# Kernel optimization log

Hardware: AMD Instinct MI355X
Metric: run time of the kernel (lower is better)

Reference implementation:

```python
import jax, jax.numpy as jnp
import numpy as np

D_MODEL = 1024
N_HEADS = 16
HEAD_DIM = D_MODEL // N_HEADS
KV_LATENT = 512
N_EXPERTS = 4
D_HIDDEN = 4 * D_MODEL
B, T = 2, 1024


def rmsnorm(x, w, eps=1e-6):
    return w * (x * jax.lax.rsqrt(jnp.mean(x * x, axis=-1, keepdims=True) + eps))


def layernorm(x, g, b, eps=1e-5):
    mu = jnp.mean(x, axis=-1, keepdims=True)
    var = jnp.mean((x - mu) ** 2, axis=-1, keepdims=True)
    return (x - mu) * jax.lax.rsqrt(var + eps) * g + b


def apply_rope(x):
    # x: [b, h, t, d], half-split RoPE as in the torch source
    t, d = x.shape[2], x.shape[3]
    half = d // 2
    pos = jnp.arange(t, dtype=x.dtype)[:, None]                      # [t,1]
    inv_freq = 1.0 / (10000.0 ** (jnp.arange(half, dtype=x.dtype) / half))
    ang = pos * inv_freq[None, :]                                    # [t,half]
    sin, cos = jnp.sin(ang), jnp.cos(ang)
    x1, x2 = x[..., :half], x[..., half:]
    return jnp.concatenate([x1 * cos - x2 * sin, x1 * sin + x2 * cos], axis=-1)


def setup_inputs() -> dict:
    key = jax.random.key(0)
    ks = jax.random.split(key, 16)
    s = lambda fan_in: 1.0 / np.sqrt(fan_in)
    return {
        "x": jax.random.normal(ks[0], (B, T, D_MODEL), jnp.float32),
        "norm1_w": jnp.ones((D_MODEL,), jnp.float32),
        "norm2_w": jnp.ones((D_MODEL,), jnp.float32),
        "Wq": jax.random.normal(ks[1], (D_MODEL, D_MODEL), jnp.float32) * s(D_MODEL),
        "Wdkv": jax.random.normal(ks[2], (KV_LATENT, D_MODEL), jnp.float32) * s(D_MODEL),
        "Wuk": jax.random.normal(ks[3], (D_MODEL, KV_LATENT), jnp.float32) * s(KV_LATENT),
        "Wuv": jax.random.normal(ks[4], (D_MODEL, KV_LATENT), jnp.float32) * s(KV_LATENT),
        "Wo": jax.random.normal(ks[5], (D_MODEL, D_MODEL), jnp.float32) * s(D_MODEL),
        "ln_g": jnp.ones((KV_LATENT,), jnp.float32),
        "ln_b": jnp.zeros((KV_LATENT,), jnp.float32),
        "gate_w": jax.random.normal(ks[6], (N_EXPERTS, D_MODEL), jnp.float32) * s(D_MODEL),
        "gate_b": jnp.zeros((N_EXPERTS,), jnp.float32),
        "W1": jax.random.normal(ks[7], (N_EXPERTS, D_HIDDEN, D_MODEL), jnp.float32) * s(D_MODEL),
        "b1": jnp.zeros((N_EXPERTS, D_HIDDEN), jnp.float32),
        "W2": jax.random.normal(ks[8], (N_EXPERTS, D_MODEL, D_HIDDEN), jnp.float32) * s(D_HIDDEN),
        "b2": jnp.zeros((N_EXPERTS, D_MODEL), jnp.float32),
    }


def mla_attention(x, Wq, Wdkv, Wuk, Wuv, Wo, ln_g, ln_b):
    b, t, _ = x.shape
    q = (x @ Wq.T).reshape(b, t, N_HEADS, HEAD_DIM).transpose(0, 2, 1, 3)  # [b,h,t,dh]
    latent = layernorm(x @ Wdkv.T, ln_g, ln_b)                             # [b,t,L]
    k = (latent @ Wuk.T).reshape(b, t, N_HEADS, HEAD_DIM).transpose(0, 2, 1, 3)
    v = (latent @ Wuv.T).reshape(b, t, N_HEADS, HEAD_DIM).transpose(0, 2, 1, 3)
    q = apply_rope(q)
    k = apply_rope(k)
    scores = jnp.einsum("bhqd,bhkd->bhqk", q, k) / np.sqrt(HEAD_DIM)
    causal = jnp.tril(jnp.ones((t, t), dtype=bool))
    scores = jnp.where(causal, scores, -jnp.inf)
    attn = jax.nn.softmax(scores, axis=-1)  # dropout is identity in eval
    out = jnp.einsum("bhqk,bhkd->bhqd", attn, v).transpose(0, 2, 1, 3).reshape(b, t, D_MODEL)
    return out @ Wo.T


def moe(x, gate_w, gate_b, W1, b1, W2, b2):
    # top-1 routing: each token goes to exactly one expert (argmax of gate)
    logits = x @ gate_w.T + gate_b                                  # [b,t,E]
    top = jnp.argmax(logits, axis=-1)                               # [b,t]
    onehot = jax.nn.one_hot(top, N_EXPERTS, dtype=x.dtype)          # [b,t,E]
    h = jax.nn.relu(jnp.einsum("btd,ehd->bteh", x, W1) + b1)        # [b,t,E,H]
    y = jnp.einsum("bteh,edh->bted", h, W2) + b2                    # [b,t,E,D]
    return jnp.einsum("bted,bte->btd", y, onehot)


def reference(x, norm1_w, norm2_w, Wq, Wdkv, Wuk, Wuv, Wo, ln_g, ln_b,
              gate_w, gate_b, W1, b1, W2, b2):
    x = x + mla_attention(rmsnorm(x, norm1_w), Wq, Wdkv, Wuk, Wuv, Wo, ln_g, ln_b)
    x = x + moe(rmsnorm(x, norm2_w), gate_w, gate_b, W1, b1, W2, b2)
    return x
```

## Files before the change

### kernel.cpp

```cpp
#include <hip/hip_runtime.h>
#include <hip/hip_bf16.h>
#include <math.h>

typedef unsigned short u16;
typedef __attribute__((ext_vector_type(4))) float floatx4;
typedef __attribute__((ext_vector_type(8))) short shortx8;

#define DEVI static __device__ __forceinline__

DEVI u16 f2b(float f) {
  union { float f; unsigned int i; } v; v.f = f;
  unsigned int x = v.i;
  return (u16)((x + 0x7fffu + ((x >> 16) & 1u)) >> 16);
}

constexpr int T_ = 1024, D_ = 1024, HD_ = 64, KV_ = 512, DH_ = 4096, M_ = 2048;
#define NEGBIG (-1e30f)

__global__ __launch_bounds__(256) void k_rms1b(const float* __restrict__ x, const float* __restrict__ w,
                                               u16* __restrict__ outb) {
  int row = blockIdx.x, tid = threadIdx.x;
  float4 v = *(const float4*)&x[(size_t)row * D_ + tid * 4];
  float ss = v.x*v.x + v.y*v.y + v.z*v.z + v.w*v.w;
  #pragma unroll
  for (int m = 32; m >= 1; m >>= 1) ss += __shfl_xor(ss, m, 64);
  __shared__ float red[4];
  if ((tid & 63) == 0) red[tid >> 6] = ss;
  __syncthreads();
  ss = red[0] + red[1] + red[2] + red[3];
  float sc = 1.0f / sqrtf(ss * (1.0f / 1024.0f) + 1e-6f);
  float4 wv = *(const float4*)&w[tid * 4];
  ushort4 ob;
  ob.x = f2b(wv.x*v.x*sc); ob.y = f2b(wv.y*v.y*sc);
  ob.z = f2b(wv.z*v.z*sc); ob.w = f2b(wv.w*v.w*sc);
  *(ushort4*)&outb[(size_t)row * D_ + tid * 4] = ob;
}

__global__ __launch_bounds__(256) void k_rms2b(const float* __restrict__ x, const float* __restrict__ w,
                                               float* __restrict__ outf, u16* __restrict__ outb) {
  int row = blockIdx.x, tid = threadIdx.x;
  float4 v = *(const float4*)&x[(size_t)row * D_ + tid * 4];
  float ss = v.x*v.x + v.y*v.y + v.z*v.z + v.w*v.w;
  #pragma unroll
  for (int m = 32; m >= 1; m >>= 1) ss += __shfl_xor(ss, m, 64);
  __shared__ float red[4];
  if ((tid & 63) == 0) red[tid >> 6] = ss;
  __syncthreads();
  ss = red[0] + red[1] + red[2] + red[3];
  float sc = 1.0f / sqrtf(ss * (1.0f / 1024.0f) + 1e-6f);
  float4 wv = *(const float4*)&w[tid * 4];
  float4 o; o.x = wv.x*v.x*sc; o.y = wv.y*v.y*sc; o.z = wv.z*v.z*sc; o.w = wv.w*v.w*sc;
  *(float4*)&outf[(size_t)row * D_ + tid * 4] = o;
  ushort4 ob; ob.x = f2b(o.x); ob.y = f2b(o.y); ob.z = f2b(o.z); ob.w = f2b(o.w);
  *(ushort4*)&outb[(size_t)row * D_ + tid * 4] = ob;
}

__global__ __launch_bounds__(256) void k_lnb(const float* __restrict__ lat, const float* __restrict__ g,
                                             const float* __restrict__ bb, u16* __restrict__ ob) {
  int row = blockIdx.x, tid = threadIdx.x;
  const float* r = lat + (size_t)row * KV_;
  float v0 = r[tid], v1 = r[tid + 256];
  float s = v0 + v1;
  #pragma unroll
  for (int m = 32; m >= 1; m >>= 1) s += __shfl_xor(s, m, 64);
  __shared__ float red[4];
  if ((tid & 63) == 0) red[tid >> 6] = s;
  __syncthreads();
  float mu = (red[0] + red[1] + red[2] + red[3]) * (1.0f / 512.0f);
  __syncthreads();
  float d0 = v0 - mu, d1 = v1 - mu;
  float ss = d0*d0 + d1*d1;
  #pragma unroll
  for (int m = 32; m >= 1; m >>= 1) ss += __shfl_xor(ss, m, 64);
  if ((tid & 63) == 0) red[tid >> 6] = ss;
  __syncthreads();
  float var = (red[0] + red[1] + red[2] + red[3]) * (1.0f / 512.0f);
  float sc = 1.0f / sqrtf(var + 1e-5f);
  ob[(size_t)row * KV_ + tid]       = f2b(d0 * sc * g[tid]       + bb[tid]);
  ob[(size_t)row * KV_ + tid + 256] = f2b(d1 * sc * g[tid + 256] + bb[tid + 256]);
}

__global__ __launch_bounds__(256) void k_cvtall(const float* __restrict__ W1, const float* __restrict__ W2,
                                                const float* __restrict__ Wq, const float* __restrict__ Wdkv,
                                                const float* __restrict__ Wuk, const float* __restrict__ Wuv,
                                                const float* __restrict__ Wo, u16* __restrict__ dst) {
  for (size_t i = (size_t)blockIdx.x * 256 + threadIdx.x; i < 9306112ull; i += (size_t)gridDim.x * 256) {
    const float* s;
    if      (i < 4194304ull) s = W1   + i * 4;
    else if (i < 8388608ull) s = W2   + (i - 4194304ull) * 4;
    else if (i < 8650752ull) s = Wq   + (i - 8388608ull) * 4;
    else if (i < 8781824ull) s = Wdkv + (i - 8650752ull) * 4;
    else if (i < 8912896ull) s = Wuk  + (i - 8781824ull) * 4;
    else if (i < 9043968ull) s = Wuv  + (i - 8912896ull) * 4;
    else                     s = Wo   + (i - 9043968ull) * 4;
    float4 f = *(const float4*)s;
    ushort4 u; u.x = f2b(f.x); u.y = f2b(f.y); u.z = f2b(f.z); u.w = f2b(f.w);
    *(ushort4*)(dst + i * 4) = u;
  }
}

template<int BF16B>
__global__ __launch_bounds__(256) void k_gemm_t(const u16* __restrict__ A, const void* __restrict__ Bp,
                                                const float* __restrict__ resid, float* __restrict__ Cf,
                                                u16* __restrict__ Cb, int N, int K) {
  int bid = blockIdx.x;
  int xcd = bid & 7, jj = bid >> 3;
  int mt = jj & 31, nt = (jj >> 5) * 8 + xcd;
  __shared__ __align__(16) u16 As[64][72];
  __shared__ __align__(16) u16 Bs[64][72];
  int tid = threadIdx.x, lane = tid & 63, wave = tid >> 6;
  int wm = (wave >> 1) * 32, wn = (wave & 1) * 32;
  int lr = tid >> 2, lc = (tid & 3) * 16;
  const u16* arow = A + (size_t)(mt * 64 + lr) * K + lc;
  const u16* browb = (const u16*)Bp + (size_t)(nt * 64 + lr) * K + lc;
  const float* browf = (const float*)Bp + (size_t)(nt * 64 + lr) * K + lc;
  floatx4 z = {0.f, 0.f, 0.f, 0.f};
  floatx4 acc00 = z, acc01 = z, acc10 = z, acc11 = z;
  int fm = lane & 15, fkq = (lane >> 4) * 8;
  uint4 ra0 = *(const uint4*)&arow[0];
  uint4 ra1 = *(const uint4*)&arow[8];
  uint4 rbA, rbB; float4 rb0, rb1, rb2, rb3;
  if constexpr (BF16B) {
    rbA = *(const uint4*)&browb[0]; rbB = *(const uint4*)&browb[8];
  } else {
    rb0 = *(const float4*)&browf[0];  rb1 = *(const float4*)&browf[4];
    rb2 = *(const float4*)&browf[8];  rb3 = *(const float4*)&browf[12];
  }
  for (int kb = 0; kb < K; kb += 64) {
    *(uint4*)&As[lr][lc]     = ra0;
    *(uint4*)&As[lr][lc + 8] = ra1;
    if constexpr (BF16B) {
      *(uint4*)&Bs[lr][lc]     = rbA;
      *(uint4*)&Bs[lr][lc + 8] = rbB;
    } else {
      ushort4 u;
      u.x = f2b(rb0.x); u.y = f2b(rb0.y); u.z = f2b(rb0.z); u.w = f2b(rb0.w); *(ushort4*)&Bs[lr][lc]      = u;
      u.x = f2b(rb1.x); u.y = f2b(rb1.y); u.z = f2b(rb1.z); u.w = f2b(rb1.w); *(ushort4*)&Bs[lr][lc + 4]  = u;
      u.x = f2b(rb2.x); u.y = f2b(rb2.y); u.z = f2b(rb2.z); u.w = f2b(rb2.w); *(ushort4*)&Bs[lr][lc + 8]  = u;
      u.x = f2b(rb3.x); u.y = f2b(rb3.y); u.z = f2b(rb3.z); u.w = f2b(rb3.w); *(ushort4*)&Bs[lr][lc + 12] = u;
    }
    __syncthreads();
    if (kb + 64 < K) {
      ra0 = *(const uint4*)&arow[kb + 64];
      ra1 = *(const uint4*)&arow[kb + 72];
      if constexpr (BF16B) {
        rbA = *(const uint4*)&browb[kb + 64]; rbB = *(const uint4*)&browb[kb + 72];
      } else {
        rb0 = *(const float4*)&browf[kb + 64]; rb1 = *(const float4*)&browf[kb + 68];
        rb2 = *(const float4*)&browf[kb + 72]; rb3 = *(const float4*)&browf[kb + 76];
      }
    }
    #pragma unroll
    for (int ks = 0; ks < 64; ks += 32) {
      shortx8 a0  = *(const shortx8*)&As[wm + fm][ks + fkq];
      shortx8 a1  = *(const shortx8*)&As[wm + 16 + fm][ks + fkq];
      shortx8 b0  = *(const shortx8*)&Bs[wn + fm][ks + fkq];
      shortx8 b1v = *(const shortx8*)&Bs[wn + 16 + fm][ks + fkq];
      acc00 = __builtin_amdgcn_mfma_f32_16x16x32_bf16(a0, b0,  acc00, 0, 0, 0);
      acc01 = __builtin_amdgcn_mfma_f32_16x16x32_bf16(a0, b1v, acc01, 0, 0, 0);
      acc10 = __builtin_amdgcn_mfma_f32_16x16x32_bf16(a1, b0,  acc10, 0, 0, 0);
      acc11 = __builtin_amdgcn_mfma_f32_16x16x32_bf16(a1, b1v, acc11, 0, 0, 0);
    }
    __syncthreads();
  }
  int q4 = (lane >> 4) * 4, cix = lane & 15;
  #pragma unroll
  for (int im = 0; im < 2; ++im) {
    #pragma unroll
    for (int rg = 0; rg < 4; ++rg) {
      int row = mt * 64 + wm + im * 16 + q4 + rg;
      #pragma unroll
      for (int in = 0; in < 2; ++in) {
        int gn = nt * 64 + wn + in * 16 + cix;
        float vv = (im == 0 ? (in == 0 ? acc00[rg] : acc01[rg]) : (in == 0 ? acc10[rg] : acc11[rg]));
        size_t idx = (size_t)row * N + gn;
        if (Cb) {
          Cb[idx] = f2b(vv);
        } else {
          if (resid) vv += resid[idx];
          Cf[idx] = vv;
        }
      }
    }
  }
}

__global__ __launch_bounds__(256) void k_rope2b(const float* __restrict__ q, const float* __restrict__ k,
                                                u16* __restrict__ qb, u16* __restrict__ kb) {
  int g = blockIdx.x * 256 + threadIdx.x;
  int j = g & 31;
  int h = (g >> 5) & 15;
  int row = g >> 9;
  int t = row & (T_ - 1);
  float p = (float)pow(10000.0, (double)j * (1.0 / 32.0));
  float ang = (float)t / p;
  float sn, cs; sincosf(ang, &sn, &cs);
  size_t base = (size_t)row * D_ + h * 64 + j;
  float x1 = q[base], x2 = q[base + 32];
  qb[base]      = f2b((x1 * cs - x2 * sn) * 0.125f);
  qb[base + 32] = f2b((x1 * sn + x2 * cs) * 0.125f);
  x1 = k[base]; x2 = k[base + 32];
  kb[base]      = f2b(x1 * cs - x2 * sn);
  kb[base + 32] = f2b(x1 * sn + x2 * cs);
}

__global__ __launch_bounds__(256) void k_fattn(const u16* __restrict__ qbp, const u16* __restrict__ kbp,
                                               const u16* __restrict__ vbp, u16* __restrict__ ob) {
  int idx = blockIdx.x, h = blockIdx.y;
  int b = idx >> 4;
  int qt = idx & 15;
  if (b) qt = 15 - qt;
  __shared__ __align__(16) u16 Qs[64][72];
  __shared__ __align__(16) u16 Ks[64][72];
  __shared__ __align__(16) u16 Vs[64][72];
  __shared__ __align__(16) u16 Ps[64][72];
  __shared__ float red1[2][64];
  __shared__ float red2[2][64];
  int tid = threadIdx.x, lane = tid & 63, wave = tid >> 6;
  int wm = (wave >> 1) * 32, wn = (wave & 1) * 32, w1 = wave & 1;
  int fm = lane & 15, fkq = (lane >> 4) * 8;
  int q4 = (lane >> 4) * 4, cix = lane & 15;
  size_t rowbase = (size_t)b * T_;
  int colbase = h * HD_;
  int q0 = qt * 64;
  int lr = tid >> 2, ld = (tid & 3) * 16;
  {
    const u16* qr = qbp + (rowbase + q0 + lr) * D_ + colbase + ld;
    *(uint4*)&Qs[lr][ld]     = *(const uint4*)&qr[0];
    *(uint4*)&Qs[lr][ld + 8] = *(const uint4*)&qr[8];
  }
  floatx4 z = {0.f, 0.f, 0.f, 0.f};
  floatx4 s[2][2], o[2][2];
  o[0][0] = z; o[0][1] = z; o[1][0] = z; o[1][1] = z;
  float m[2][4], l[2][4], f_[2][4];
  #pragma unroll
  for (int im = 0; im < 2; ++im)
    #pragma unroll
    for (int rg = 0; rg < 4; ++rg) { m[im][rg] = NEGBIG; l[im][rg] = 0.f; }
  for (int kt = 0; kt <= qt; ++kt) {
    __syncthreads();
    {
      const u16* kr = kbp + (rowbase + kt * 64 + lr) * D_ + colbase + ld;
      *(uint4*)&Ks[lr][ld]     = *(const uint4*)&kr[0];
      *(uint4*)&Ks[lr][ld + 8] = *(const uint4*)&kr[8];
      const u16* vr = vbp + (rowbase + kt * 64 + lr) * D_ + colbase + ld;
      #pragma unroll
      for (int c = 0; c < 16; ++c) Vs[ld + c][lr] = vr[c];
    }
    __syncthreads();
    s[0][0] = z; s[0][1] = z; s[1][0] = z; s[1][1] = z;
    #pragma unroll
    for (int ks = 0; ks < 64; ks += 32) {
      shortx8 a0  = *(const shortx8*)&Qs[wm + fm][ks + fkq];
      shortx8 a1  = *(const shortx8*)&Qs[wm + 16 + fm][ks + fkq];
      shortx8 b0  = *(const shortx8*)&Ks[wn + fm][ks + fkq];
      shortx8 b1v = *(const shortx8*)&Ks[wn + 16 + fm][ks + fkq];
      s[0][0] = __builtin_amdgcn_mfma_f32_16x16x32_bf16(a0, b0,  s[0][0], 0, 0, 0);
      s[0][1] = __builtin_amdgcn_mfma_f32_16x16x32_bf16(a0, b1v, s[0][1], 0, 0, 0);
      s[1][0] = __builtin_amdgcn_mfma_f32_16x16x32_bf16(a1, b0,  s[1][0], 0, 0, 0);
      s[1][1] = __builtin_amdgcn_mfma_f32_16x16x32_bf16(a1, b1v, s[1][1], 0, 0, 0);
    }
    if (kt == qt) {
      #pragma unroll
      for (int im = 0; im < 2; ++im)
        #pragma unroll
        for (int rg = 0; rg < 4; ++rg) {
          int r = wm + im * 16 + q4 + rg;
          #pragma unroll
          for (int in = 0; in < 2; ++in)
            if (wn + in * 16 + cix > r) s[im][in][rg] = NEGBIG;
        }
    }
    #pragma unroll
    for (int im = 0; im < 2; ++im)
      #pragma unroll
      for (int rg = 0; rg < 4; ++rg) {
        float pm = fmaxf(s[im][0][rg], s[im][1][rg]);
        #pragma unroll
        for (int mk = 8; mk >= 1; mk >>= 1) pm = fmaxf(pm, __shfl_xor(pm, mk, 64));
        if (cix == 0) red1[w1][wm + im * 16 + q4 + rg] = pm;
        f_[im][rg] = pm;
      }
    __syncthreads();
    #pragma unroll
    for (int im = 0; im < 2; ++im)
      #pragma unroll
      for (int rg = 0; rg < 4; ++rg) {
        int r = wm + im * 16 + q4 + rg;
        float mx = fmaxf(f_[im][rg], red1[w1 ^ 1][r]);
        float mn = fmaxf(m[im][rg], mx);
        float f = __expf(m[im][rg] - mn);
        m[im][rg] = mn;
        float p0 = __expf(s[im][0][rg] - mn);
        float p1 = __expf(s[im][1][rg] - mn);
        float ss = p0 + p1;
        #pragma unroll
        for (int mk = 8; mk >= 1; mk >>= 1) ss += __shfl_xor(ss, mk, 64);
        if (cix == 0) red2[w1][r] = ss;
        Ps[r][wn + cix]      = f2b(p0);
        Ps[r][wn + 16 + cix] = f2b(p1);
        l[im][rg] *= f;
        o[im][0][rg] *= f;
        o[im][1][rg] *= f;
      }
    __syncthreads();
    #pragma unroll
    for (int im = 0; im < 2; ++im)
      #pragma unroll
      for (int rg = 0; rg < 4; ++rg) {
        int r = wm + im * 16 + q4 + rg;
        l[im][rg] += red2[0][r] + red2[1][r];
      }
    #pragma unroll
    for (int ks = 0; ks < 64; ks += 32) {
      shortx8 a0  = *(const shortx8*)&Ps[wm + fm][ks + fkq];
      shortx8 a1  = *(const shortx8*)&Ps[wm + 16 + fm][ks + fkq];
      shortx8 b0  = *(const shortx8*)&Vs[wn + fm][ks + fkq];
      shortx8 b1v = *(const shortx8*)&Vs[wn + 16 + fm][ks + fkq];
      o[0][0] = __builtin_amdgcn_mfma_f32_16x16x32_bf16(a0, b0,  o[0][0], 0, 0, 0);
      o[0][1] = __builtin_amdgcn_mfma_f32_16x16x32_bf16(a0, b1v, o[0][1], 0, 0, 0);
      o[1][0] = __builtin_amdgcn_mfma_f32_16x16x32_bf16(a1, b0,  o[1][0], 0, 0, 0);
      o[1][1] = __builtin_amdgcn_mfma_f32_16x16x32_bf16(a1, b1v, o[1][1], 0, 0, 0);
    }
  }
  #pragma unroll
  for (int im = 0; im < 2; ++im)
    #pragma unroll
    for (int rg = 0; rg < 4; ++rg) {
      int r = wm + im * 16 + q4 + rg;
      float inv = 1.0f / l[im][rg];
      size_t base = (rowbase + q0 + r) * D_ + colbase;
      ob[base + wn + cix]      = f2b(o[im][0][rg] * inv);
      ob[base + wn + 16 + cix] = f2b(o[im][1][rg] * inv);
    }
}

__global__ __launch_bounds__(256) void k_init(int* cnt) { if (threadIdx.x < 4) cnt[threadIdx.x] = 0; }

__global__ __launch_bounds__(256) void k_gate(const float* __restrict__ h2, const float* __restrict__ gw,
                                              const float* __restrict__ gb, int* __restrict__ expert,
                                              int* __restrict__ cnt) {
  int wid = threadIdx.x >> 6, lane = threadIdx.x & 63;
  int t = blockIdx.x * 4 + wid;
  const float* hr = h2 + (size_t)t * D_;
  float a0 = 0, a1 = 0, a2 = 0, a3 = 0;
  for (int c = lane; c < D_; c += 64) {
    float xv = hr[c];
    a0 += xv * gw[c];
    a1 += xv * gw[D_ + c];
    a2 += xv * gw[2 * D_ + c];
    a3 += xv * gw[3 * D_ + c];
  }
  #pragma unroll
  for (int m = 32; m >= 1; m >>= 1) {
    a0 += __shfl_xor(a0, m, 64); a1 += __shfl_xor(a1, m, 64);
    a2 += __shfl_xor(a2, m, 64); a3 += __shfl_xor(a3, m, 64);
  }
  if (lane == 0) {
    float l0 = a0 + gb[0], l1 = a1 + gb[1], l2 = a2 + gb[2], l3 = a3 + gb[3];
    int best = 0; float bv = l0;
    if (l1 > bv) { bv = l1; best = 1; }
    if (l2 > bv) { bv = l2; best = 2; }
    if (l3 > bv) { bv = l3; best = 3; }
    expert[t] = best;
    atomicAdd(&cnt[best], 1);
  }
}

__global__ __launch_bounds__(256) void k_scatter(const int* __restrict__ expert, const int* __restrict__ cnt,
                                                 int* __restrict__ off, int* __restrict__ sorted) {
  __shared__ int cur[4];
  if (threadIdx.x == 0) {
    int o0 = 0, o1 = cnt[0], o2 = o1 + cnt[1], o3 = o2 + cnt[2];
    off[0] = o0; off[1] = o1; off[2] = o2; off[3] = o3;
    cur[0] = o0; cur[1] = o1; cur[2] = o2; cur[3] = o3;
  }
  __syncthreads();
  for (int t = threadIdx.x; t < M_; t += 256) {
    int e = expert[t];
    int p = atomicAdd(&cur[e], 1);
    sorted[p] = t;
  }
}

template<int BF16B>
__global__ __launch_bounds__(256) void k_moe1_t(const u16* __restrict__ A, const void* __restrict__ W1p,
                                                const float* __restrict__ b1, const int* __restrict__ cnt,
                                                const int* __restrict__ off, const int* __restrict__ sorted,
                                                u16* __restrict__ hbuf) {
  int bid = blockIdx.x;
  int xcd = bid & 7, jj = bid >> 3;
  int mt = jj & 31, combo = (jj >> 5) * 8 + xcd;
  int e = combo >> 6, nt = combo & 63;
  int rem = cnt[e] - mt * 64;
  if (rem <= 0) return;
  __shared__ __align__(16) u16 As[64][72];
  __shared__ __align__(16) u16 Bs[64][72];
  int tid = threadIdx.x, lane = tid & 63, wave = tid >> 6;
  int wm = (wave >> 1) * 32, wn = (wave & 1) * 32;
  int lr = tid >> 2, lc = (tid & 3) * 16;
  int rr = lr < rem ? lr : rem - 1;
  const u16* arow = A + (size_t)sorted[off[e] + mt * 64 + rr] * D_ + lc;
  const u16* browb = (const u16*)W1p + (size_t)e * DH_ * D_ + (size_t)(nt * 64 + lr) * D_ + lc;
  const float* browf = (const float*)W1p + (size_t)e * DH_ * D_ + (size_t)(nt * 64 + lr) * D_ + lc;
  floatx4 z = {0.f, 0.f, 0.f, 0.f};
  floatx4 acc00 = z, acc01 = z, acc10 = z, acc11 = z;
  int fm = lane & 15, fkq = (lane >> 4) * 8;
  uint4 ra0 = *(const uint4*)&arow[0];
  uint4 ra1 = *(const uint4*)&arow[8];
  uint4 rbA, rbB; float4 rb0, rb1, rb2, rb3;
  if constexpr (BF16B) {
    rbA = *(const uint4*)&browb[0]; rbB = *(const uint4*)&browb[8];
  } else {
    rb0 = *(const float4*)&browf[0];  rb1 = *(const float4*)&browf[4];
    rb2 = *(const float4*)&browf[8];  rb3 = *(const float4*)&browf[12];
  }
  for (int kb = 0; kb < D_; kb += 64) {
    *(uint4*)&As[lr][lc]     = ra0;
    *(uint4*)&As[lr][lc + 8] = ra1;
    if constexpr (BF16B) {
      *(uint4*)&Bs[lr][lc]     = rbA;
      *(uint4*)&Bs[lr][lc + 8] = rbB;
    } else {
      ushort4 u;
      u.x = f2b(rb0.x); u.y = f2b(rb0.y); u.z = f2b(rb0.z); u.w = f2b(rb0.w); *(ushort4*)&Bs[lr][lc]      = u;
      u.x = f2b(rb1.x); u.y = f2b(rb1.y); u.z = f2b(rb1.z); u.w = f2b(rb1.w); *(ushort4*)&Bs[lr][lc + 4]  = u;
      u.x = f2b(rb2.x); u.y = f2b(rb2.y); u.z = f2b(rb2.z); u.w = f2b(rb2.w); *(ushort4*)&Bs[lr][lc + 8]  = u;
      u.x = f2b(rb3.x); u.y = f2b(rb3.y); u.z = f2b(rb3.z); u.w = f2b(rb3.w); *(ushort4*)&Bs[lr][lc + 12] = u;
    }
    __syncthreads();
    if (kb + 64 < D_) {
      ra0 = *(const uint4*)&arow[kb + 64];
      ra1 = *(const uint4*)&arow[kb + 72];
      if constexpr (BF16B) {
        rbA = *(const uint4*)&browb[kb + 64]; rbB = *(const uint4*)&browb[kb + 72];
      } else {
        rb0 = *(const float4*)&browf[kb + 64]; rb1 = *(const float4*)&browf[kb + 68];
        rb2 = *(const float4*)&browf[kb + 72]; rb3 = *(const float4*)&browf[kb + 76];
      }
    }
    #pragma unroll
    for (int ks = 0; ks < 64; ks += 32) {
      shortx8 a0  = *(const shortx8*)&As[wm + fm][ks + fkq];
      shortx8 a1  = *(const shortx8*)&As[wm + 16 + fm][ks + fkq];
      shortx8 b0  = *(const shortx8*)&Bs[wn + fm][ks + fkq];
      shortx8 b1v = *(const shortx8*)&Bs[wn + 16 + fm][ks + fkq];
      acc00 = __builtin_amdgcn_mfma_f32_16x16x32_bf16(a0, b0,  acc00, 0, 0, 0);
      acc01 = __builtin_amdgcn_mfma_f32_16x16x32_bf16(a0, b1v, acc01, 0, 0, 0);
      acc10 = __builtin_amdgcn_mfma_f32_16x16x32_bf16(a1, b0,  acc10, 0, 0, 0);
      acc11 = __builtin_amdgcn_mfma_f32_16x16x32_bf16(a1, b1v, acc11, 0, 0, 0);
    }
    __syncthreads();
  }
  int q4 = (lane >> 4) * 4, cix = lane & 15;
  #pragma unroll
  for (int im = 0; im < 2; ++im) {
    #pragma unroll
    for (int rg = 0; rg < 4; ++rg) {
      int ml = wm + im * 16 + q4 + rg;
      if (ml >= rem) continue;
      size_t grow = (size_t)(off[e] + mt * 64 + ml);
      #pragma unroll
      for (int in = 0; in < 2; ++in) {
        int gn = nt * 64 + wn + in * 16 + cix;
        float vv = (im == 0 ? (in == 0 ? acc00[rg] : acc01[rg]) : (in == 0 ? acc10[rg] : acc11[rg]));
        vv += b1[e * DH_ + gn];
        hbuf[grow * DH_ + gn] = f2b(fmaxf(vv, 0.f));
      }
    }
  }
}

template<int BF16B>
__global__ __launch_bounds__(256) void k_moe2_t(const u16* __restrict__ hbuf, const void* __restrict__ W2p,
                                                const float* __restrict__ b2w, const float* __restrict__ x1f,
                                                const int* __restrict__ cnt, const int* __restrict__ off,
                                                const int* __restrict__ sorted, float* __restrict__ out) {
  int bid = blockIdx.x;
  int xcd = bid & 7, jj = bid >> 3;
  int mt = jj & 31, combo = (jj >> 5) * 8 + xcd;
  int e = combo >> 4, nt = combo & 15;
  int rem = cnt[e] - mt * 64;
  if (rem <= 0) return;
  __shared__ __align__(16) u16 As[64][72];
  __shared__ __align__(16) u16 Bs[64][72];
  int tid = threadIdx.x, lane = tid & 63, wave = tid >> 6;
  int wm = (wave >> 1) * 32, wn = (wave & 1) * 32;
  int lr = tid >> 2, lc = (tid & 3) * 16;
  int rr = lr < rem ? lr : rem - 1;
  const u16* arow = hbuf + (size_t)(off[e] + mt * 64 + rr) * DH_ + lc;
  const u16* browb = (const u16*)W2p + (size_t)e * D_ * DH_ + (size_t)(nt * 64 + lr) * DH_ + lc;
  const float* browf = (const float*)W2p + (size_t)e * D_ * DH_ + (size_t)(nt * 64 + lr) * DH_ + lc;
  floatx4 z = {0.f, 0.f, 0.f, 0.f};
  floatx4 acc00 = z, acc01 = z, acc10 = z, acc11 = z;
  int fm = lane & 15, fkq = (lane >> 4) * 8;
  uint4 ra0 = *(const uint4*)&arow[0];
  uint4 ra1 = *(const uint4*)&arow[8];
  uint4 rbA, rbB; float4 rb0, rb1, rb2, rb3;
  if constexpr (BF16B) {
    rbA = *(const uint4*)&browb[0]; rbB = *(const uint4*)&browb[8];
  } else {
    rb0 = *(const float4*)&browf[0];  rb1 = *(const float4*)&browf[4];
    rb2 = *(const float4*)&browf[8];  rb3 = *(const float4*)&browf[12];
  }
  for (int kb = 0; kb < DH_; kb += 64) {
    *(uint4*)&As[lr][lc]     = ra0;
    *(uint4*)&As[lr][lc + 8] = ra1;
    if constexpr (BF16B) {
      *(uint4*)&Bs[lr][lc]     = rbA;
      *(uint4*)&Bs[lr][lc + 8] = rbB;
    } else {
      ushort4 u;
      u.x = f2b(rb0.x); u.y = f2b(rb0.y); u.z = f2b(rb0.z); u.w = f2b(rb0.w); *(ushort4*)&Bs[lr][lc]      = u;
      u.x = f2b(rb1.x); u.y = f2b(rb1.y); u.z = f2b(rb1.z); u.w = f2b(rb1.w); *(ushort4*)&Bs[lr][lc + 4]  = u;
      u.x = f2b(rb2.x); u.y = f2b(rb2.y); u.z = f2b(rb2.z); u.w = f2b(rb2.w); *(ushort4*)&Bs[lr][lc + 8]  = u;
      u.x = f2b(rb3.x); u.y = f2b(rb3.y); u.z = f2b(rb3.z); u.w = f2b(rb3.w); *(ushort4*)&Bs[lr][lc + 12] = u;
    }
    __syncthreads();
    if (kb + 64 < DH_) {
      ra0 = *(const uint4*)&arow[kb + 64];
      ra1 = *(const uint4*)&arow[kb + 72];
      if constexpr (BF16B) {
        rbA = *(const uint4*)&browb[kb + 64]; rbB = *(const uint4*)&browb[kb + 72];
      } else {
        rb0 = *(const float4*)&browf[kb + 64]; rb1 = *(const float4*)&browf[kb + 68];
        rb2 = *(const float4*)&browf[kb + 72]; rb3 = *(const float4*)&browf[kb + 76];
      }
    }
    #pragma unroll
    for (int ks = 0; ks < 64; ks += 32) {
      shortx8 a0  = *(const shortx8*)&As[wm + fm][ks + fkq];
      shortx8 a1  = *(const shortx8*)&As[wm + 16 + fm][ks + fkq];
      shortx8 b0  = *(const shortx8*)&Bs[wn + fm][ks + fkq];
      shortx8 b1v = *(const shortx8*)&Bs[wn + 16 + fm][ks + fkq];
      acc00 = __builtin_amdgcn_mfma_f32_16x16x32_bf16(a0, b0,  acc00, 0, 0, 0);
      acc01 = __builtin_amdgcn_mfma_f32_16x16x32_bf16(a0, b1v, acc01, 0, 0, 0);
      acc10 = __builtin_amdgcn_mfma_f32_16x16x32_bf16(a1, b0,  acc10, 0, 0, 0);
      acc11 = __builtin_amdgcn_mfma_f32_16x16x32_bf16(a1, b1v, acc11, 0, 0, 0);
    }
    __syncthreads();
  }
  int q4 = (lane >> 4) * 4, cix = lane & 15;
  #pragma unroll
  for (int im = 0; im < 2; ++im) {
    #pragma unroll
    for (int rg = 0; rg < 4; ++rg) {
      int ml = wm + im * 16 + q4 + rg;
      if (ml >= rem) continue;
      int tok = sorted[off[e] + mt * 64 + ml];
      #pragma unroll
      for (int in = 0; in < 2; ++in) {
        int gn = nt * 64 + wn + in * 16 + cix;
        float vv = (im == 0 ? (in == 0 ? acc00[rg] : acc01[rg]) : (in == 0 ? acc10[rg] : acc11[rg]));
        out[(size_t)tok * D_ + gn] = vv + b2w[e * D_ + gn] + x1f[(size_t)tok * D_ + gn];
      }
    }
  }
}

__global__ __launch_bounds__(256) void k_moe2s(const u16* __restrict__ hbuf, const u16* __restrict__ W2b,
                                               const int* __restrict__ cnt, const int* __restrict__ off,
                                               float* __restrict__ pbuf) {
  int bid = blockIdx.x;
  int xcd = bid & 7, jj = bid >> 3;
  int mt = jj & 31;
  int combo = (jj >> 5) * 8 + xcd;
  int ks = combo & 1, ec = combo >> 1;
  int e = ec >> 4, nt = ec & 15;
  int rem = cnt[e] - mt * 64;
  if (rem <= 0) return;
  const int KS = DH_ / 2;
  int k0 = ks * KS;
  __shared__ __align__(16) u16 As[64][72];
  __shared__ __align__(16) u16 Bs[64][72];
  int tid = threadIdx.x, lane = tid & 63, wave = tid >> 6;
  int wm = (wave >> 1) * 32, wn = (wave & 1) * 32;
  int lr = tid >> 2, lc = (tid & 3) * 16;
  int rr = lr < rem ? lr : rem - 1;
  const u16* arow = hbuf + (size_t)(off[e] + mt * 64 + rr) * DH_ + k0 + lc;
  const u16* brow = W2b + (size_t)e * D_ * DH_ + (size_t)(nt * 64 + lr) * DH_ + k0 + lc;
  floatx4 z = {0.f, 0.f, 0.f, 0.f};
  floatx4 acc00 = z, acc01 = z, acc10 = z, acc11 = z;
  int fm = lane & 15, fkq = (lane >> 4) * 8;
  uint4 ra0 = *(const uint4*)&arow[0];
  uint4 ra1 = *(const uint4*)&arow[8];
  uint4 rbA = *(const uint4*)&brow[0];
  uint4 rbB = *(const uint4*)&brow[8];
  for (int kb = 0; kb < KS; kb += 64) {
    *(uint4*)&As[lr][lc]     = ra0;
    *(uint4*)&As[lr][lc + 8] = ra1;
    *(uint4*)&Bs[lr][lc]     = rbA;
    *(uint4*)&Bs[lr][lc + 8] = rbB;
    __syncthreads();
    if (kb + 64 < KS) {
      ra0 = *(const uint4*)&arow[kb + 64];
      ra1 = *(const uint4*)&arow[kb + 72];
      rbA = *(const uint4*)&brow[kb + 64];
      rbB = *(const uint4*)&brow[kb + 72];
    }
    #pragma unroll
    for (int kk = 0; kk < 64; kk += 32) {
      shortx8 a0  = *(const shortx8*)&As[wm + fm][kk + fkq];
      shortx8 a1  = *(const shortx8*)&As[wm + 16 + fm][kk + fkq];
      shortx8 b0  = *(const shortx8*)&Bs[wn + fm][kk + fkq];
      shortx8 b1v = *(const shortx8*)&Bs[wn + 16 + fm][kk + fkq];
      acc00 = __builtin_amdgcn_mfma_f32_16x16x32_bf16(a0, b0,  acc00, 0, 0, 0);
      acc01 = __builtin_amdgcn_mfma_f32_16x16x32_bf16(a0, b1v, acc01, 0, 0, 0);
      acc10 = __builtin_amdgcn_mfma_f32_16x16x32_bf16(a1, b0,  acc10, 0, 0, 0);
      acc11 = __builtin_amdgcn_mfma_f32_16x16x32_bf16(a1, b1v, acc11, 0, 0, 0);
    }
    __syncthreads();
  }
  float* pb = pbuf + (size_t)ks * M_ * D_;
  int q4 = (lane >> 4) * 4, cix = lane & 15;
  #pragma unroll
  for (int im = 0; im < 2; ++im) {
    #pragma unroll
    for (int rg = 0; rg < 4; ++rg) {
      int ml = wm + im * 16 + q4 + rg;
      if (ml >= rem) continue;
      size_t srow = (size_t)(off[e] + mt * 64 + ml);
      #pragma unroll
      for (int in = 0; in < 2; ++in) {
        int gn = nt * 64 + wn + in * 16 + cix;
        float vv = (im == 0 ? (in == 0 ? acc00[rg] : acc01[rg]) : (in == 0 ? acc10[rg] : acc11[rg]));
        pb[srow * D_ + gn] = vv;
      }
    }
  }
}

__global__ __launch_bounds__(256) void k_moered(const float* __restrict__ pbuf, const float* __restrict__ b2w,
                                                const float* __restrict__ x1f, const int* __restrict__ off,
                                                const int* __restrict__ sorted, float* __restrict__ out) {
  int r = blockIdx.x, tid = threadIdx.x;
  int tok = sorted[r];
  int e = (r >= off[3]) ? 3 : (r >= off[2]) ? 2 : (r >= off[1]) ? 1 : 0;
  size_t c = (size_t)tid * 4;
  float4 a = *(const float4*)&pbuf[(size_t)r * D_ + c];
  float4 b = *(const float4*)&pbuf[(size_t)M_ * D_ + (size_t)r * D_ + c];
  float4 bb = *(const float4*)&b2w[(size_t)e * D_ + c];
  float4 xr = *(const float4*)&x1f[(size_t)tok * D_ + c];
  float4 o;
  o.x = a.x + b.x + bb.x + xr.x;
  o.y = a.y + b.y + bb.y + xr.y;
  o.z = a.z + b.z + bb.z + xr.z;
  o.w = a.w + b.w + bb.w + xr.w;
  *(float4*)&out[(size_t)tok * D_ + c] = o;
}

extern "C" void kernel_launch(void* const* d_in, const int* in_sizes, int n_in,
                              void* d_out, int out_size, void* d_ws, size_t ws_size,
                              hipStream_t stream) {
  int map[16];
  for (int i = 0; i < 16; ++i) map[i] = i;
  if (n_in == 16 && in_sizes[0] == 16777216) {
    const int mm[16] = {15, 13, 14, 4, 2, 5, 6, 3, 12, 11, 10, 9, 0, 7, 1, 8};
    for (int i = 0; i < 16; ++i) map[i] = mm[i];
  } else if (n_in == 16 && in_sizes[0] == 4096) {
    for (int i = 0; i < 16; ++i) map[i] = 15 - i;
  }
  const float* x    = (const float*)d_in[map[0]];
  const float* n1w  = (const float*)d_in[map[1]];
  const float* n2w  = (const float*)d_in[map[2]];
  const float* Wq   = (const float*)d_in[map[3]];
  const float* Wdkv = (const float*)d_in[map[4]];
  const float* Wuk  = (const float*)d_in[map[5]];
  const float* Wuv  = (const float*)d_in[map[6]];
  const float* Wo   = (const float*)d_in[map[7]];
  const float* lng  = (const float*)d_in[map[8]];
  const float* lnb  = (const float*)d_in[map[9]];
  const float* gw   = (const float*)d_in[map[10]];
  const float* gb   = (const float*)d_in[map[11]];
  const float* W1   = (const float*)d_in[map[12]];
  const float* b1   = (const float*)d_in[map[13]];
  const float* W2   = (const float*)d_in[map[14]];
  const float* b2w  = (const float*)d_in[map[15]];
  float* out = (float*)d_out;
  char* ws = (char*)d_ws;
  const size_t MB = 1ull << 20;
  float* qf   = (float*)(ws + 0);
  float* x1f  = (float*)(ws + 0);
  float* kf   = (float*)(ws + 8 * MB);
  u16*   hbuf = (u16*)(ws + 8 * MB);
  float* latf = (float*)(ws + 16 * MB);
  u16*   qb   = (u16*)(ws + 16 * MB);
  u16*   h1b  = (u16*)(ws + 20 * MB);
  u16*   kb   = (u16*)(ws + 20 * MB);
  u16*   latb = (u16*)(ws + 24 * MB);
  float* h2f  = (float*)(ws + 24 * MB);
  u16*   vb   = (u16*)(ws + 26 * MB);
  u16*   ab   = (u16*)(ws + 30 * MB);
  u16*   h2b  = (u16*)(ws + 32 * MB);
  float* pbuf = (float*)(ws + 24 * MB);

  bool big = ws_size >= (107ull * MB + (64ull << 10));
  u16* wb = (u16*)(ws + 36 * MB);
  u16* W1b   = wb;
  u16* W2b   = wb + 16777216;
  u16* Wqb   = wb + 33554432;
  u16* Wdkvb = wb + 34603008;
  u16* Wukb  = wb + 35127296;
  u16* Wuvb  = wb + 35651584;
  u16* Wob   = wb + 36175872;
  int* cnt    = (int*)(ws + (big ? 107 * MB : 36 * MB));
  int* off    = cnt + 8;
  int* expert = cnt + 16;
  int* sorted = expert + 2048;

  if (big) {
    k_cvtall<<<2048, 256, 0, stream>>>(W1, W2, Wq, Wdkv, Wuk, Wuv, Wo, wb);
    k_rms1b<<<2048, 256, 0, stream>>>(x, n1w, h1b);
    k_gemm_t<1><<<512, 256, 0, stream>>>(h1b, Wqb, nullptr, qf, nullptr, 1024, 1024);
    k_gemm_t<1><<<256, 256, 0, stream>>>(h1b, Wdkvb, nullptr, latf, nullptr, 512, 1024);
    k_lnb<<<2048, 256, 0, stream>>>(latf, lng, lnb, latb);
    k_gemm_t<1><<<512, 256, 0, stream>>>(latb, Wukb, nullptr, kf, nullptr, 1024, 512);
    k_gemm_t<1><<<512, 256, 0, stream>>>(latb, Wuvb, nullptr, nullptr, vb, 1024, 512);
    k_rope2b<<<4096, 256, 0, stream>>>(qf, kf, qb, kb);
    k_fattn<<<dim3(32, 16), 256, 0, stream>>>(qb, kb, vb, ab);
    k_gemm_t<1><<<512, 256, 0, stream>>>(ab, Wob, x, x1f, nullptr, 1024, 1024);
    k_rms2b<<<2048, 256, 0, stream>>>(x1f, n2w, h2f, h2b);
    k_init<<<1, 64, 0, stream>>>(cnt);
    k_gate<<<512, 256, 0, stream>>>(h2f, gw, gb, expert, cnt);
    k_scatter<<<1, 256, 0, stream>>>(expert, cnt, off, sorted);
    k_moe1_t<1><<<8192, 256, 0, stream>>>(h2b, W1b, b1, cnt, off, sorted, hbuf);
    k_moe2s<<<4096, 256, 0, stream>>>(hbuf, W2b, cnt, off, pbuf);
    k_moered<<<2048, 256, 0, stream>>>(pbuf, b2w, x1f, off, sorted, out);
  } else {
    k_rms1b<<<2048, 256, 0, stream>>>(x, n1w, h1b);
    k_gemm_t<0><<<512, 256, 0, stream>>>(h1b, Wq, nullptr, qf, nullptr, 1024, 1024);
    k_gemm_t<0><<<256, 256, 0, stream>>>(h1b, Wdkv, nullptr, latf, nullptr, 512, 1024);
    k_lnb<<<2048, 256, 0, stream>>>(latf, lng, lnb, latb);
    k_gemm_t<0><<<512, 256, 0, stream>>>(latb, Wuk, nullptr, kf, nullptr, 1024, 512);
    k_gemm_t<0><<<512, 256, 0, stream>>>(latb, Wuv, nullptr, nullptr, vb, 1024, 512);
    k_rope2b<<<4096, 256, 0, stream>>>(qf, kf, qb, kb);
    k_fattn<<<dim3(32, 16), 256, 0, stream>>>(qb, kb, vb, ab);
    k_gemm_t<0><<<512, 256, 0, stream>>>(ab, Wo, x, x1f, nullptr, 1024, 1024);
    k_rms2b<<<2048, 256, 0, stream>>>(x1f, n2w, h2f, h2b);
    k_init<<<1, 64, 0, stream>>>(cnt);
    k_gate<<<512, 256, 0, stream>>>(h2f, gw, gb, expert, cnt);
    k_scatter<<<1, 256, 0, stream>>>(expert, cnt, off, sorted);
    k_moe1_t<0><<<8192, 256, 0, stream>>>(h2b, W1, b1, cnt, off, sorted, hbuf);
    k_moe2_t<0><<<2048, 256, 0, stream>>>(hbuf, W2, b2w, x1f, cnt, off, sorted, out);
  }
}
```

Baseline: 468.7 us.

## Give each wave full key rows in flash attention and prefetch K/V

Changes the flash-attention warp split so each of the four waves owns 16 query rows across all 64 keys, instead of a 2x2 quadrant split. Row max and row sum now come from in-wave shuffles alone, which removes the shared-memory reduction buffers and two block-wide barriers per key tile. Global K/V loads for the next tile are issued into registers before the current tile's compute, overlapping memory latency with MFMA work. The cost is more registers per thread for the prefetched tile, and the V transpose into shared memory now happens from registers.

```diff
diff --git a/kernel.cpp b/kernel.cpp
--- a/kernel.cpp
+++ b/kernel.cpp
@@ -214,12 +214,10 @@
   __shared__ __align__(16) u16 Ks[64][72];
   __shared__ __align__(16) u16 Vs[64][72];
   __shared__ __align__(16) u16 Ps[64][72];
-  __shared__ float red1[2][64];
-  __shared__ float red2[2][64];
   int tid = threadIdx.x, lane = tid & 63, wave = tid >> 6;
-  int wm = (wave >> 1) * 32, wn = (wave & 1) * 32, w1 = wave & 1;
   int fm = lane & 15, fkq = (lane >> 4) * 8;
   int q4 = (lane >> 4) * 4, cix = lane & 15;
+  int w16 = wave * 16;
   size_t rowbase = (size_t)b * T_;
   int colbase = h * HD_;
   int q0 = qt * 64;
@@ -230,109 +228,89 @@
     *(uint4*)&Qs[lr][ld + 8] = *(const uint4*)&qr[8];
   }
   floatx4 z = {0.f, 0.f, 0.f, 0.f};
-  floatx4 s[2][2], o[2][2];
-  o[0][0] = z; o[0][1] = z; o[1][0] = z; o[1][1] = z;
-  float m[2][4], l[2][4], f_[2][4];
-  #pragma unroll
-  for (int im = 0; im < 2; ++im)
-    #pragma unroll
-    for (int rg = 0; rg < 4; ++rg) { m[im][rg] = NEGBIG; l[im][rg] = 0.f; }
+  floatx4 s[4], o[4];
+  o[0] = z; o[1] = z; o[2] = z; o[3] = z;
+  float m[4], l[4];
+  #pragma unroll
+  for (int rg = 0; rg < 4; ++rg) { m[rg] = NEGBIG; l[rg] = 0.f; }
+  const u16* kr = kbp + (rowbase + lr) * D_ + colbase + ld;
+  const u16* vr = vbp + (rowbase + lr) * D_ + colbase + ld;
+  uint4 rk0 = *(const uint4*)&kr[0], rk1 = *(const uint4*)&kr[8];
+  uint4 rv0 = *(const uint4*)&vr[0], rv1 = *(const uint4*)&vr[8];
   for (int kt = 0; kt <= qt; ++kt) {
     __syncthreads();
+    *(uint4*)&Ks[lr][ld]     = rk0;
+    *(uint4*)&Ks[lr][ld + 8] = rk1;
     {
-      const u16* kr = kbp + (rowbase + kt * 64 + lr) * D_ + colbase + ld;
-      *(uint4*)&Ks[lr][ld]     = *(const uint4*)&kr[0];
-      *(uint4*)&Ks[lr][ld + 8] = *(const uint4*)&kr[8];
-      const u16* vr = vbp + (rowbase + kt * 64 + lr) * D_ + colbase + ld;
-      #pragma unroll
-      for (int c = 0; c < 16; ++c) Vs[ld + c][lr] = vr[c];
-    }
-    __syncthreads();
-    s[0][0] = z; s[0][1] = z; s[1][0] = z; s[1][1] = z;
+      union { uint4 v4[2]; u16 e[16]; } vv;
+      vv.v4[0] = rv0; vv.v4[1] = rv1;
+      #pragma unroll
+      for (int c = 0; c < 16; ++c) Vs[ld + c][lr] = vv.e[c];
+    }
+    __syncthreads();
+    if (kt < qt) {
+      kr += 64 * D_; vr += 64 * D_;
+      rk0 = *(const uint4*)&kr[0]; rk1 = *(const uint4*)&kr[8];
+      rv0 = *(const uint4*)&vr[0]; rv1 = *(const uint4*)&vr[8];
+    }
+    s[0] = z; s[1] = z; s[2] = z; s[3] = z;
     #pragma unroll
     for (int ks = 0; ks < 64; ks += 32) {
-      shortx8 a0  = *(const shortx8*)&Qs[wm + fm][ks + fkq];
-      shortx8 a1  = *(const shortx8*)&Qs[wm + 16 + fm][ks + fkq];
-      shortx8 b0  = *(const shortx8*)&Ks[wn + fm][ks + fkq];
-      shortx8 b1v = *(const shortx8*)&Ks[wn + 16 + fm][ks + fkq];
-      s[0][0] = __builtin_amdgcn_mfma_f32_16x16x32_bf16(a0, b0,  s[0][0], 0, 0, 0);
-      s[0][1] = __builtin_amdgcn_mfma_f32_16x16x32_bf16(a0, b1v, s[0][1], 0, 0, 0);
-      s[1][0] = __builtin_amdgcn_mfma_f32_16x16x32_bf16(a1, b0,  s[1][0], 0, 0, 0);
-      s[1][1] = __builtin_amdgcn_mfma_f32_16x16x32_bf16(a1, b1v, s[1][1], 0, 0, 0);
+      shortx8 a = *(const shortx8*)&Qs[w16 + fm][ks + fkq];
+      #pragma unroll
+      for (int nb = 0; nb < 4; ++nb) {
+        shortx8 bb = *(const shortx8*)&Ks[nb * 16 + fm][ks + fkq];
+        s[nb] = __builtin_amdgcn_mfma_f32_16x16x32_bf16(a, bb, s[nb], 0, 0, 0);
+      }
     }
     if (kt == qt) {
       #pragma unroll
-      for (int im = 0; im < 2; ++im)
+      for (int nb = 0; nb < 4; ++nb)
         #pragma unroll
-        for (int rg = 0; rg < 4; ++rg) {
-          int r = wm + im * 16 + q4 + rg;
-          #pragma unroll
-          for (int in = 0; in < 2; ++in)
-            if (wn + in * 16 + cix > r) s[im][in][rg] = NEGBIG;
-        }
-    }
-    #pragma unroll
-    for (int im = 0; im < 2; ++im)
-      #pragma unroll
-      for (int rg = 0; rg < 4; ++rg) {
-        float pm = fmaxf(s[im][0][rg], s[im][1][rg]);
-        #pragma unroll
-        for (int mk = 8; mk >= 1; mk >>= 1) pm = fmaxf(pm, __shfl_xor(pm, mk, 64));
-        if (cix == 0) red1[w1][wm + im * 16 + q4 + rg] = pm;
-        f_[im][rg] = pm;
-      }
-    __syncthreads();
-    #pragma unroll
-    for (int im = 0; im < 2; ++im)
-      #pragma unroll
-      for (int rg = 0; rg < 4; ++rg) {
-        int r = wm + im * 16 + q4 + rg;
-        float mx = fmaxf(f_[im][rg], red1[w1 ^ 1][r]);
-        float mn = fmaxf(m[im][rg], mx);
-        float f = __expf(m[im][rg] - mn);
-        m[im][rg] = mn;
-        float p0 = __expf(s[im][0][rg] - mn);
-        float p1 = __expf(s[im][1][rg] - mn);
-        float ss = p0 + p1;
-        #pragma unroll
-        for (int mk = 8; mk >= 1; mk >>= 1) ss += __shfl_xor(ss, mk, 64);
-        if (cix == 0) red2[w1][r] = ss;
-        Ps[r][wn + cix]      = f2b(p0);
-        Ps[r][wn + 16 + cix] = f2b(p1);
-        l[im][rg] *= f;
-        o[im][0][rg] *= f;
-        o[im][1][rg] *= f;
-      }
-    __syncthreads();
-    #pragma unroll
-    for (int im = 0; im < 2; ++im)
-      #pragma unroll
-      for (int rg = 0; rg < 4; ++rg) {
-        int r = wm + im * 16 + q4 + rg;
-        l[im][rg] += red2[0][r] + red2[1][r];
-      }
+        for (int rg = 0; rg < 4; ++rg)
+          if (nb * 16 + cix > w16 + q4 + rg) s[nb][rg] = NEGBIG;
+    }
+    #pragma unroll
+    for (int rg = 0; rg < 4; ++rg) {
+      float mx = fmaxf(fmaxf(s[0][rg], s[1][rg]), fmaxf(s[2][rg], s[3][rg]));
+      #pragma unroll
+      for (int mk = 8; mk >= 1; mk >>= 1) mx = fmaxf(mx, __shfl_xor(mx, mk, 64));
+      float mn = fmaxf(m[rg], mx);
+      float f = __expf(m[rg] - mn);
+      m[rg] = mn;
+      float p0 = __expf(s[0][rg] - mn);
+      float p1 = __expf(s[1][rg] - mn);
+      float p2 = __expf(s[2][rg] - mn);
+      float p3 = __expf(s[3][rg] - mn);
+      float rs = (p0 + p1) + (p2 + p3);
+      #pragma unroll
+      for (int mk = 8; mk >= 1; mk >>= 1) rs += __shfl_xor(rs, mk, 64);
+      l[rg] = l[rg] * f + rs;
+      o[0][rg] *= f; o[1][rg] *= f; o[2][rg] *= f; o[3][rg] *= f;
+      int prow = w16 + q4 + rg;
+      Ps[prow][cix]      = f2b(p0);
+      Ps[prow][16 + cix] = f2b(p1);
+      Ps[prow][32 + cix] = f2b(p2);
+      Ps[prow][48 + cix] = f2b(p3);
+    }
     #pragma unroll
     for (int ks = 0; ks < 64; ks += 32) {
-      shortx8 a0  = *(const shortx8*)&Ps[wm + fm][ks + fkq];
-      shortx8 a1  = *(const shortx8*)&Ps[wm + 16 + fm][ks + fkq];
-      shortx8 b0  = *(const shortx8*)&Vs[wn + fm][ks + fkq];
-      shortx8 b1v = *(const shortx8*)&Vs[wn + 16 + fm][ks + fkq];
-      o[0][0] = __builtin_amdgcn_mfma_f32_16x16x32_bf16(a0, b0,  o[0][0], 0, 0, 0);
-      o[0][1] = __builtin_amdgcn_mfma_f32_16x16x32_bf16(a0, b1v, o[0][1], 0, 0, 0);
-      o[1][0] = __builtin_amdgcn_mfma_f32_16x16x32_bf16(a1, b0,  o[1][0], 0, 0, 0);
-      o[1][1] = __builtin_amdgcn_mfma_f32_16x16x32_bf16(a1, b1v, o[1][1], 0, 0, 0);
-    }
-  }
-  #pragma unroll
-  for (int im = 0; im < 2; ++im)
-    #pragma unroll
-    for (int rg = 0; rg < 4; ++rg) {
-      int r = wm + im * 16 + q4 + rg;
-      float inv = 1.0f / l[im][rg];
-      size_t base = (rowbase + q0 + r) * D_ + colbase;
-      ob[base + wn + cix]      = f2b(o[im][0][rg] * inv);
-      ob[base + wn + 16 + cix] = f2b(o[im][1][rg] * inv);
-    }
+      shortx8 a = *(const shortx8*)&Ps[w16 + fm][ks + fkq];
+      #pragma unroll
+      for (int db = 0; db < 4; ++db) {
+        shortx8 bb = *(const shortx8*)&Vs[db * 16 + fm][ks + fkq];
+        o[db] = __builtin_amdgcn_mfma_f32_16x16x32_bf16(a, bb, o[db], 0, 0, 0);
+      }
+    }
+  }
+  #pragma unroll
+  for (int rg = 0; rg < 4; ++rg) {
+    float inv = 1.0f / l[rg];
+    size_t base = (rowbase + q0 + w16 + q4 + rg) * D_ + colbase;
+    #pragma unroll
+    for (int db = 0; db < 4; ++db)
+      ob[base + db * 16 + cix] = f2b(o[db][rg] * inv);
+  }
 }
 
 __global__ __launch_bounds__(256) void k_init(int* cnt) { if (threadIdx.x < 4) cnt[threadIdx.x] = 0; }
```

Result: faster. 436.8 us (-6.8%).
